# Optimization experiments

Measured on AMD Instinct MI355X. Metric: run time of the kernel, lower is better.

## Reference

```python
import jax, jax.numpy as jnp
import numpy as np

B, T, D_IN, H, D_OUT = 64, 512, 512, 1024, 512

def setup_inputs() -> dict:
    key = jax.random.key(0)
    ks = jax.random.split(key, 8)
    s = 0.02  # weight init scale to keep gates in a sane range
    return {
        "x": jax.random.normal(ks[0], (B, T, D_IN), jnp.float32),
        "hx": jax.random.normal(ks[1], (B, H), jnp.float32) * 0.1,
        "cx": jax.random.normal(ks[2], (B, H), jnp.float32) * 0.1,
        "yx": jax.nn.softmax(jax.random.normal(ks[3], (B, D_OUT), jnp.float32), axis=-1),
        "Wi": jax.random.normal(ks[4], (4 * H, D_IN), jnp.float32) * s,
        "bi": jnp.zeros((4 * H,), jnp.float32),
        "Wh": jax.random.normal(ks[5], (4 * H, H), jnp.float32) * s,
        "bh": jnp.zeros((4 * H,), jnp.float32),
        "Wp": jax.random.normal(ks[6], (4 * H, D_OUT), jnp.float32) * s,
        "bp": jnp.zeros((4 * H,), jnp.float32),
        "Wo": jax.random.normal(ks[7], (D_OUT, H), jnp.float32) * s,
        "bo": jnp.zeros((D_OUT,), jnp.float32),
    }

def reference(x, hx, cx, yx, Wi, bi, Wh, bh, Wp, bp, Wo, bo):
    # Precompute input projections for all timesteps: [T, B, 4H]
    xg = jnp.einsum("btd,gd->tbg", x, Wi) + bi

    def step(carry, xg_t):
        h, c, y = carry
        gates = xg_t + h @ Wh.T + bh + y @ Wp.T + bp  # [B, 4H]
        i_g, f_g, g_g, o_g = jnp.split(gates, 4, axis=-1)
        i_g = jax.nn.sigmoid(i_g)
        f_g = jax.nn.sigmoid(f_g)
        g_g = jnp.tanh(g_g)
        o_g = jax.nn.sigmoid(o_g)
        c_new = f_g * c + i_g * g_g
        h_new = o_g * jnp.tanh(c_new)
        y_new = jax.nn.softmax(h_new @ Wo.T + bo, axis=-1)  # softmax feedback
        return (h_new, c_new, y_new), (h_new, y_new)

    (hT, cT, yT), (h_seq, y_seq) = jax.lax.scan(step, (hx, cx, yx), xg)
    output = jnp.transpose(h_seq, (1, 0, 2))       # [B, T, H]   (batch_first)
    output_peep = jnp.transpose(y_seq, (1, 0, 2))  # [B, T, D_OUT]
    return output, output_peep, hT, cT, yT
```

## Files before the change

### kernel.cpp

```cpp
#include <hip/hip_runtime.h>
#include <math.h>


typedef __bf16 bf16;
typedef bf16  bf16x8 __attribute__((ext_vector_type(8)));
typedef float f32x4  __attribute__((ext_vector_type(4)));
typedef unsigned long long u64;
typedef unsigned int u32;

#define B_    64
#define T_    512
#define DIN_  512
#define H_    1024
#define DOUT_ 512
#define NBLK  256
#define NTHR  512
#define GBLK  64
#define GROWS 16

__device__ __forceinline__ bf16x8 ld8f(const float* __restrict__ p) {
  const float4 a = *(const float4*)p;
  const float4 b = *(const float4*)(p + 4);
  bf16x8 r;
  r[0]=(bf16)a.x; r[1]=(bf16)a.y; r[2]=(bf16)a.z; r[3]=(bf16)a.w;
  r[4]=(bf16)b.x; r[5]=(bf16)b.y; r[6]=(bf16)b.z; r[7]=(bf16)b.w;
  return r;
}

__device__ __forceinline__ float sigm(float x){ return 1.f/(1.f+__expf(-x)); }

__device__ __forceinline__ void st_u64(void* p, u64 v) {
  __hip_atomic_store((u64*)p, v, __ATOMIC_RELAXED, __HIP_MEMORY_SCOPE_AGENT);
}
__device__ __forceinline__ u64 ld_u64(const void* p) {
  return __hip_atomic_load((const u64*)p, __ATOMIC_RELAXED, __HIP_MEMORY_SCOPE_AGENT);
}
__device__ __forceinline__ void st_u32(void* p, u32 v) {
  __hip_atomic_store((u32*)p, v, __ATOMIC_RELAXED, __HIP_MEMORY_SCOPE_AGENT);
}
__device__ __forceinline__ u32 ld_u32(const void* p) {
  return __hip_atomic_load((const u32*)p, __ATOMIC_RELAXED, __HIP_MEMORY_SCOPE_AGENT);
}
__device__ __forceinline__ void st_f32(float* p, float v) {
  __hip_atomic_store(p, v, __ATOMIC_RELAXED, __HIP_MEMORY_SCOPE_AGENT);
}
__device__ __forceinline__ void at_addf(float* p, float v) {
  __hip_atomic_fetch_add(p, v, __ATOMIC_RELAXED, __HIP_MEMORY_SCOPE_AGENT);
}
__device__ __forceinline__ bf16x8 ldh16(const bf16* p) {
  union { u64 q[2]; bf16x8 v; } u;
  u.q[0] = ld_u64(p);
  u.q[1] = ld_u64(p + 4);
  return u.v;
}

__global__ __launch_bounds__(NTHR, 2)
void lstm_kernel(const float* __restrict__ x,  const float* __restrict__ hx,
                 const float* __restrict__ cx, const float* __restrict__ yx,
                 const float* __restrict__ Wi, const float* __restrict__ bi,
                 const float* __restrict__ Wh, const float* __restrict__ bh,
                 const float* __restrict__ Wp, const float* __restrict__ bp,
                 const float* __restrict__ Wo, const float* __restrict__ bo,
                 float* __restrict__ out, char* __restrict__ ws) {
  u32*   flags  = (u32*)ws;
  float* logits = (float*)(ws + 32768);
  bf16*  hbuf   = (bf16*)(ws + 32768 + 4*3*GROWS*DOUT_*4);

  float* out_h  = out;
  float* out_y  = out + (size_t)B_*T_*H_;
  float* out_hT = out_y + (size_t)B_*T_*DOUT_;
  float* out_cT = out_hT + B_*H_;
  float* out_yT = out_cT + B_*H_;

  const int tid  = threadIdx.x;
  const int bid  = blockIdx.x;
  const int g    = bid & 3;
  const int n    = bid >> 2;
  const int w    = tid >> 6;
  const int lane = tid & 63;
  const int quad = lane >> 4;
  const int ln15 = lane & 15;
  const int r0   = g * GROWS;

  u32*   gfl = flags + (size_t)(g * GBLK) * 32;
  float* lgt = logits + (size_t)g * 3 * GROWS * DOUT_;

  __shared__ float lred[8][16][66];
  __shared__ bf16  hstage[16][16];
  __shared__ float lds_rs[2][16];

  bf16* h0 = hbuf;
  bf16* h1 = hbuf + (size_t)B_*H_;

  bf16x8 wfrag[8][4];
  {
    #pragma unroll
    for (int ks = 0; ks < 8; ++ks) {
      #pragma unroll
      for (int ns = 0; ns < 4; ++ns) {
        const int grow = ns*H_ + n*16 + ln15;
        const int kabs = w*256 + ks*32 + quad*8;
        const float* p;
        if      (w < 2) p = Wi + (size_t)grow * DIN_  + kabs;
        else if (w < 6) p = Wh + (size_t)grow * H_    + (kabs - 512);
        else            p = Wp + (size_t)grow * DOUT_ + (kabs - 1536);
        wfrag[ks][ns] = ld8f(p);
      }
    }
  }

  bf16x8 wofrag2[4];
  {
    bf16x8 z;
    #pragma unroll
    for (int j = 0; j < 8; ++j) z[j] = (bf16)0.f;
    #pragma unroll
    for (int m = 0; m < 4; ++m) {
      if (quad < 2)
        wofrag2[m] = ld8f(Wo + (size_t)(w*64 + m*16 + ln15)*H_ + n*16 + quad*8);
      else
        wofrag2[m] = z;
    }
  }

  const int crow = (tid >> 4) & 15;
  const int chl  = tid & 15;
  const int cb   = r0 + crow;
  const int ccol = n*16 + chl;
  float c = 0.f;
  float bias4[4];
  if (tid < 256) {
    c = cx[(size_t)cb * H_ + ccol];
    #pragma unroll
    for (int gg = 0; gg < 4; ++gg) {
      const int grow = gg*H_ + ccol;
      bias4[gg] = bi[grow] + bh[grow] + bp[grow];
    }
  }

  float bo_mine = 0.f;
  if (tid < 128) bo_mine = bo[(n*128 + tid) & (DOUT_ - 1)];

  {
    const int idx = n * NTHR + tid;
    if (idx < GROWS*H_/2) {
      const int row = idx >> 9, c2 = (idx & 511) * 2;
      const float* hp = hx + (size_t)(r0 + row)*H_ + c2;
      union { u32 q; bf16 h[2]; } u;
      u.h[0] = (bf16)hp[0]; u.h[1] = (bf16)hp[1];
      st_u32(h0 + (size_t)(r0 + row)*H_ + c2, u.q);
    }
    if (tid < 128) st_f32(lgt + n*128 + tid, bo_mine);
  }

  u32 ep = 1;
  {
    asm volatile("s_waitcnt vmcnt(0)" ::: "memory");
    __syncthreads();
    if (tid == 0) st_u32(gfl + (size_t)n * 32, ep);
    if (tid < GBLK) {
      const u32* f = gfl + (size_t)tid * 32;
      while (ld_u32(f) < ep) __builtin_amdgcn_s_sleep(1);
    }
    __syncthreads();
  }

  for (int t = 0; t < T_; ++t) {
    bf16*       hbR = (t & 1) ? h1 : h0;
    bf16*       hbW = (t & 1) ? h0 : h1;
    const float* lgtPrev = lgt + (size_t)((t + 2) % 3) * GROWS * DOUT_;
    float*       lgtCur  = lgt + (size_t)(t % 3)       * GROWS * DOUT_;
    float*       lgtNext = lgt + (size_t)((t + 1) % 3) * GROWS * DOUT_;

    f32x4 acc[4];
    #pragma unroll
    for (int j = 0; j < 4; ++j) acc[j] = f32x4{0.f, 0.f, 0.f, 0.f};

    if (w < 2) {
      const float* base = x + ((size_t)(r0 + ln15)*T_ + t)*DIN_ + w*256 + quad*8;
      #pragma unroll
      for (int ks = 0; ks < 8; ++ks) {
        const bf16x8 a = ld8f(base + ks*32);
        #pragma unroll
        for (int ns = 0; ns < 4; ++ns)
          acc[ns] = __builtin_amdgcn_mfma_f32_16x16x32_bf16(a, wfrag[ks][ns], acc[ns], 0,0,0);
      }
    } else if (w < 6) {
      const bf16* base = hbR + (size_t)(r0 + ln15)*H_ + (w-2)*256 + quad*8;
      #pragma unroll
      for (int ks = 0; ks < 8; ++ks) {
        const bf16x8 a = ldh16(base + ks*32);
        #pragma unroll
        for (int ns = 0; ns < 4; ++ns)
          acc[ns] = __builtin_amdgcn_mfma_f32_16x16x32_bf16(a, wfrag[ks][ns], acc[ns], 0,0,0);
      }
    } else {
      float rs = 0.f;
      #pragma unroll
      for (int ks = 0; ks < 8; ++ks) {
        const int col = (w-6)*256 + ks*32 + quad*8;
        float pv[8];
        if (t == 0) {
          const float* yp = yx + (size_t)(r0 + ln15)*DOUT_ + col;
          const float4 a4 = *(const float4*)yp;
          const float4 b4 = *(const float4*)(yp + 4);
          pv[0]=a4.x; pv[1]=a4.y; pv[2]=a4.z; pv[3]=a4.w;
          pv[4]=b4.x; pv[5]=b4.y; pv[6]=b4.z; pv[7]=b4.w;
        } else {
          const float* pp = lgtPrev + ln15*DOUT_ + col;
          #pragma unroll
          for (int u2 = 0; u2 < 4; ++u2) {
            union { u64 q; float f[2]; } ua; ua.q = ld_u64(pp + u2*2);
            pv[u2*2]   = __expf(ua.f[0]);
            pv[u2*2+1] = __expf(ua.f[1]);
          }
        }
        bf16x8 a;
        #pragma unroll
        for (int j = 0; j < 8; ++j) { rs += pv[j]; a[j] = (bf16)pv[j]; }
        #pragma unroll
        for (int ns = 0; ns < 4; ++ns)
          acc[ns] = __builtin_amdgcn_mfma_f32_16x16x32_bf16(a, wfrag[ks][ns], acc[ns], 0,0,0);
      }
      rs += __shfl_xor(rs, 16);
      rs += __shfl_xor(rs, 32);
      if (quad == 0) lds_rs[w-6][ln15] = rs;
    }

    #pragma unroll
    for (int ns = 0; ns < 4; ++ns)
      #pragma unroll
      for (int r = 0; r < 4; ++r)
        lred[w][quad*4 + r][ns*16 + ln15] = acc[ns][r];
    __syncthreads();

    float rinv_y = 1.f;
    if (w >= 6 && t > 0)
      rinv_y = 1.f / (lds_rs[0][ln15] + lds_rs[1][ln15]);

    float hn = 0.f;
    if (tid < 256) {
      const float rsum = lds_rs[0][crow] + lds_rs[1][crow];
      const float rinv = (t == 0) ? 1.f : 1.f / rsum;
      float v[4];
      #pragma unroll
      for (int gg = 0; gg < 4; ++gg) {
        const int cl = gg*16 + chl;
        const float s05 = lred[0][crow][cl] + lred[1][crow][cl] + lred[2][crow][cl]
                        + lred[3][crow][cl] + lred[4][crow][cl] + lred[5][crow][cl];
        const float se  = lred[6][crow][cl] + lred[7][crow][cl];
        v[gg] = s05 + se * rinv + bias4[gg];
      }
      const float ig = sigm(v[0]);
      const float fg = sigm(v[1]);
      const float gv = tanhf(v[2]);
      const float og = sigm(v[3]);
      c = fg * c + ig * gv;
      hn = og * tanhf(c);
      hstage[crow][chl] = (bf16)hn;
    }
    __syncthreads();

    {
      bf16x8 a2;
      #pragma unroll
      for (int j = 0; j < 8; ++j) a2[j] = (bf16)0.f;
      if (quad < 2) a2 = *(const bf16x8*)&hstage[ln15][quad*8];
      #pragma unroll
      for (int m = 0; m < 4; ++m) {
        f32x4 d = f32x4{0.f, 0.f, 0.f, 0.f};
        d = __builtin_amdgcn_mfma_f32_16x16x32_bf16(a2, wofrag2[m], d, 0,0,0);
        #pragma unroll
        for (int r = 0; r < 4; ++r)
          at_addf(lgtCur + (quad*4 + r)*DOUT_ + w*64 + m*16 + ln15, d[r]);
      }
    }

    if (tid < 64) {
      const int row = tid >> 2, c4 = (tid & 3) * 4;
      union { u64 q; bf16 h[4]; } u;
      #pragma unroll
      for (int j = 0; j < 4; ++j) u.h[j] = hstage[row][c4 + j];
      st_u64(hbW + (size_t)(r0 + row)*H_ + n*16 + c4, u.q);
    }
    if (tid < 128) st_f32(lgtNext + n*128 + tid, bo_mine);

    asm volatile("s_waitcnt vmcnt(0)" ::: "memory");
    __syncthreads();
    ++ep;
    if (tid == 0) st_u32(gfl + (size_t)n * 32, ep);

    if (tid < 256) {
      out_h[((size_t)cb * T_ + t) * H_ + ccol] = hn;
      if (t == T_ - 1) {
        out_hT[(size_t)cb * H_ + ccol] = hn;
        out_cT[(size_t)cb * H_ + ccol] = c;
      }
    }
    if (w >= 6 && n < 8 && t > 0) {
      const int col = (w-6)*256 + n*32 + quad*8;
      const float* pp = lgtPrev + ln15*DOUT_ + col;
      float* oy = out_y + ((size_t)(r0 + ln15)*T_ + (t - 1))*DOUT_ + col;
      #pragma unroll
      for (int u2 = 0; u2 < 4; ++u2) {
        union { u64 q; float f[2]; } ua; ua.q = ld_u64(pp + u2*2);
        oy[u2*2]   = __expf(ua.f[0]) * rinv_y;
        oy[u2*2+1] = __expf(ua.f[1]) * rinv_y;
      }
    }

    if (tid < GBLK) {
      const u32* f = gfl + (size_t)tid * 32;
      while (ld_u32(f) < ep) __builtin_amdgcn_s_sleep(1);
    }
    __syncthreads();
  }

  if (n < 8) {
    const float* lp = lgt + (size_t)((T_ + 2) % 3) * GROWS * DOUT_;
    if (w >= 6) {
      float rs = 0.f;
      #pragma unroll
      for (int ks = 0; ks < 8; ++ks) {
        const int col = (w-6)*256 + ks*32 + quad*8;
        const float* pp = lp + ln15*DOUT_ + col;
        #pragma unroll
        for (int u2 = 0; u2 < 4; ++u2) {
          union { u64 q; float f[2]; } ua; ua.q = ld_u64(pp + u2*2);
          rs += __expf(ua.f[0]) + __expf(ua.f[1]);
        }
      }
      rs += __shfl_xor(rs, 16);
      rs += __shfl_xor(rs, 32);
      if (quad == 0) lds_rs[w-6][ln15] = rs;
    }
    __syncthreads();
    if (w >= 6) {
      const float rinv = 1.f / (lds_rs[0][ln15] + lds_rs[1][ln15]);
      const int col = (w-6)*256 + n*32 + quad*8;
      const float* pp = lp + ln15*DOUT_ + col;
      float* oy  = out_y  + ((size_t)(r0 + ln15)*T_ + (T_ - 1))*DOUT_ + col;
      float* oyT = out_yT + (size_t)(r0 + ln15)*DOUT_ + col;
      #pragma unroll
      for (int u2 = 0; u2 < 4; ++u2) {
        union { u64 q; float f[2]; } ua; ua.q = ld_u64(pp + u2*2);
        const float y0 = __expf(ua.f[0]) * rinv;
        const float y1 = __expf(ua.f[1]) * rinv;
        oy[u2*2] = y0;  oy[u2*2+1] = y1;
        oyT[u2*2] = y0; oyT[u2*2+1] = y1;
      }
    }
  }
}

extern "C" void kernel_launch(void* const* d_in, const int* in_sizes, int n_in,
                              void* d_out, int out_size, void* d_ws, size_t ws_size,
                              hipStream_t stream) {
  (void)hipMemsetAsync(d_ws, 0, 32768, stream);
  hipLaunchKernelGGL(lstm_kernel, dim3(NBLK), dim3(NTHR), 0, stream,
                     (const float*)d_in[0],  (const float*)d_in[1],
                     (const float*)d_in[2],  (const float*)d_in[3],
                     (const float*)d_in[4],  (const float*)d_in[5],
                     (const float*)d_in[6],  (const float*)d_in[7],
                     (const float*)d_in[8],  (const float*)d_in[9],
                     (const float*)d_in[10], (const float*)d_in[11],
                     (float*)d_out, (char*)d_ws);
}
```

Before: 7.253 ms.

## Replace atomic logit accumulation with second barrier phase and bf16 exp buffer

Drops the per-step float atomic adds into a shared logits buffer. Each step now has two grid-group barriers: after h is published, every block computes a full-K slice of the output projection for 8 logit columns, exponentiates it, and writes bf16 exp values for the next step's peephole input. The x input projection for the next step is computed early, after the second barrier, to take it off the critical path. The second barrier adds a sync per step, and storing exp values as bf16 instead of fp32 logits lowers the precision of the softmax numerator and its sum.

Measured after the change: 6.384 ms. 1.14x faster.

```diff
diff --git a/kernel.cpp b/kernel.cpp
--- a/kernel.cpp
+++ b/kernel.cpp
@@ -41,12 +41,6 @@
 __device__ __forceinline__ u32 ld_u32(const void* p) {
   return __hip_atomic_load((const u32*)p, __ATOMIC_RELAXED, __HIP_MEMORY_SCOPE_AGENT);
 }
-__device__ __forceinline__ void st_f32(float* p, float v) {
-  __hip_atomic_store(p, v, __ATOMIC_RELAXED, __HIP_MEMORY_SCOPE_AGENT);
-}
-__device__ __forceinline__ void at_addf(float* p, float v) {
-  __hip_atomic_fetch_add(p, v, __ATOMIC_RELAXED, __HIP_MEMORY_SCOPE_AGENT);
-}
 __device__ __forceinline__ bf16x8 ldh16(const bf16* p) {
   union { u64 q[2]; bf16x8 v; } u;
   u.q[0] = ld_u64(p);
@@ -62,9 +56,10 @@
                  const float* __restrict__ Wp, const float* __restrict__ bp,
                  const float* __restrict__ Wo, const float* __restrict__ bo,
                  float* __restrict__ out, char* __restrict__ ws) {
-  u32*   flags  = (u32*)ws;
-  float* logits = (float*)(ws + 32768);
-  bf16*  hbuf   = (bf16*)(ws + 32768 + 4*3*GROWS*DOUT_*4);
+  u32*  flagsA = (u32*)ws;
+  u32*  flagsB = (u32*)(ws + 32768);
+  bf16* hbuf   = (bf16*)(ws + 65536);
+  bf16* ebuf   = (bf16*)(ws + 65536 + (size_t)2*B_*H_*2);
 
   float* out_h  = out;
   float* out_y  = out + (size_t)B_*T_*H_;
@@ -82,8 +77,8 @@
   const int ln15 = lane & 15;
   const int r0   = g * GROWS;
 
-  u32*   gfl = flags + (size_t)(g * GBLK) * 32;
-  float* lgt = logits + (size_t)g * 3 * GROWS * DOUT_;
+  u32* gflA = flagsA + (size_t)(g * GBLK) * 32;
+  u32* gflB = flagsB + (size_t)(g * GBLK) * 32;
 
   __shared__ float lred[8][16][66];
   __shared__ bf16  hstage[16][16];
@@ -109,19 +104,13 @@
     }
   }
 
-  bf16x8 wofrag2[4];
+  bf16x8 wofrag[4];
   {
-    bf16x8 z;
-    #pragma unroll
-    for (int j = 0; j < 8; ++j) z[j] = (bf16)0.f;
-    #pragma unroll
-    for (int m = 0; m < 4; ++m) {
-      if (quad < 2)
-        wofrag2[m] = ld8f(Wo + (size_t)(w*64 + m*16 + ln15)*H_ + n*16 + quad*8);
-      else
-        wofrag2[m] = z;
-    }
-  }
+    #pragma unroll
+    for (int ks = 0; ks < 4; ++ks)
+      wofrag[ks] = ld8f(Wo + (size_t)(n*8 + (ln15 & 7))*H_ + w*128 + ks*32 + quad*8);
+  }
+  const float bo_reg = bo[n*8 + (tid & 7)];
 
   const int crow = (tid >> 4) & 15;
   const int chl  = tid & 15;
@@ -138,9 +127,6 @@
     }
   }
 
-  float bo_mine = 0.f;
-  if (tid < 128) bo_mine = bo[(n*128 + tid) & (DOUT_ - 1)];
-
   {
     const int idx = n * NTHR + tid;
     if (idx < GROWS*H_/2) {
@@ -150,77 +136,80 @@
       u.h[0] = (bf16)hp[0]; u.h[1] = (bf16)hp[1];
       st_u32(h0 + (size_t)(r0 + row)*H_ + c2, u.q);
     }
-    if (tid < 128) st_f32(lgt + n*128 + tid, bo_mine);
-  }
-
-  u32 ep = 1;
-  {
-    asm volatile("s_waitcnt vmcnt(0)" ::: "memory");
-    __syncthreads();
-    if (tid == 0) st_u32(gfl + (size_t)n * 32, ep);
+  }
+
+  f32x4 acc[4];
+  if (w < 2) {
+    #pragma unroll
+    for (int j = 0; j < 4; ++j) acc[j] = f32x4{0.f, 0.f, 0.f, 0.f};
+    const float* base = x + (size_t)(r0 + ln15)*T_*DIN_ + w*256 + quad*8;
+    #pragma unroll
+    for (int ks = 0; ks < 8; ++ks) {
+      const bf16x8 a = ld8f(base + ks*32);
+      #pragma unroll
+      for (int ns = 0; ns < 4; ++ns)
+        acc[ns] = __builtin_amdgcn_mfma_f32_16x16x32_bf16(a, wfrag[ks][ns], acc[ns], 0,0,0);
+    }
+  }
+
+  asm volatile("s_waitcnt vmcnt(0)" ::: "memory");
+  __syncthreads();
+  if (tid == 0) st_u32(gflA + (size_t)n * 32, 1u);
+
+  for (int t = 0; t < T_; ++t) {
+    const bf16* hbR = (t & 1) ? h1 : h0;
+    bf16*       hbW = (t & 1) ? h0 : h1;
+    const bf16* EbR = ebuf + (size_t)((t + 2) % 3) * B_ * DOUT_;
+    bf16*       EbW = ebuf + (size_t)(t % 3)       * B_ * DOUT_;
+
     if (tid < GBLK) {
-      const u32* f = gfl + (size_t)tid * 32;
-      while (ld_u32(f) < ep) __builtin_amdgcn_s_sleep(1);
-    }
-    __syncthreads();
-  }
-
-  for (int t = 0; t < T_; ++t) {
-    bf16*       hbR = (t & 1) ? h1 : h0;
-    bf16*       hbW = (t & 1) ? h0 : h1;
-    const float* lgtPrev = lgt + (size_t)((t + 2) % 3) * GROWS * DOUT_;
-    float*       lgtCur  = lgt + (size_t)(t % 3)       * GROWS * DOUT_;
-    float*       lgtNext = lgt + (size_t)((t + 1) % 3) * GROWS * DOUT_;
-
-    f32x4 acc[4];
-    #pragma unroll
-    for (int j = 0; j < 4; ++j) acc[j] = f32x4{0.f, 0.f, 0.f, 0.f};
-
-    if (w < 2) {
-      const float* base = x + ((size_t)(r0 + ln15)*T_ + t)*DIN_ + w*256 + quad*8;
+      const u32* f = gflA + (size_t)tid * 32;
+      while (ld_u32(f) < (u32)(t + 1)) __builtin_amdgcn_s_sleep(1);
+    }
+    __syncthreads();
+
+    float rinv_y = 1.f;
+
+    if (w >= 2 && w < 6) {
+      #pragma unroll
+      for (int j = 0; j < 4; ++j) acc[j] = f32x4{0.f, 0.f, 0.f, 0.f};
+      const bf16* base = hbR + (size_t)(r0 + ln15)*H_ + (w-2)*256 + quad*8;
       #pragma unroll
       for (int ks = 0; ks < 8; ++ks) {
-        const bf16x8 a = ld8f(base + ks*32);
+        const bf16x8 a = ldh16(base + ks*32);
         #pragma unroll
         for (int ns = 0; ns < 4; ++ns)
           acc[ns] = __builtin_amdgcn_mfma_f32_16x16x32_bf16(a, wfrag[ks][ns], acc[ns], 0,0,0);
       }
-    } else if (w < 6) {
-      const bf16* base = hbR + (size_t)(r0 + ln15)*H_ + (w-2)*256 + quad*8;
-      #pragma unroll
-      for (int ks = 0; ks < 8; ++ks) {
-        const bf16x8 a = ldh16(base + ks*32);
-        #pragma unroll
-        for (int ns = 0; ns < 4; ++ns)
-          acc[ns] = __builtin_amdgcn_mfma_f32_16x16x32_bf16(a, wfrag[ks][ns], acc[ns], 0,0,0);
-      }
-    } else {
+    } else if (w >= 6) {
+      #pragma unroll
+      for (int j = 0; j < 4; ++j) acc[j] = f32x4{0.f, 0.f, 0.f, 0.f};
       float rs = 0.f;
-      #pragma unroll
-      for (int ks = 0; ks < 8; ++ks) {
-        const int col = (w-6)*256 + ks*32 + quad*8;
-        float pv[8];
-        if (t == 0) {
-          const float* yp = yx + (size_t)(r0 + ln15)*DOUT_ + col;
-          const float4 a4 = *(const float4*)yp;
-          const float4 b4 = *(const float4*)(yp + 4);
-          pv[0]=a4.x; pv[1]=a4.y; pv[2]=a4.z; pv[3]=a4.w;
-          pv[4]=b4.x; pv[5]=b4.y; pv[6]=b4.z; pv[7]=b4.w;
-        } else {
-          const float* pp = lgtPrev + ln15*DOUT_ + col;
+      if (t == 0) {
+        const float* yp0 = yx + (size_t)(r0 + ln15)*DOUT_ + (w-6)*256 + quad*8;
+        #pragma unroll
+        for (int ks = 0; ks < 8; ++ks) {
+          const float4 a4 = *(const float4*)(yp0 + ks*32);
+          const float4 b4 = *(const float4*)(yp0 + ks*32 + 4);
+          bf16x8 a;
+          a[0]=(bf16)a4.x; a[1]=(bf16)a4.y; a[2]=(bf16)a4.z; a[3]=(bf16)a4.w;
+          a[4]=(bf16)b4.x; a[5]=(bf16)b4.y; a[6]=(bf16)b4.z; a[7]=(bf16)b4.w;
+          rs += a4.x+a4.y+a4.z+a4.w+b4.x+b4.y+b4.z+b4.w;
           #pragma unroll
-          for (int u2 = 0; u2 < 4; ++u2) {
-            union { u64 q; float f[2]; } ua; ua.q = ld_u64(pp + u2*2);
-            pv[u2*2]   = __expf(ua.f[0]);
-            pv[u2*2+1] = __expf(ua.f[1]);
-          }
+          for (int ns = 0; ns < 4; ++ns)
+            acc[ns] = __builtin_amdgcn_mfma_f32_16x16x32_bf16(a, wfrag[ks][ns], acc[ns], 0,0,0);
         }
-        bf16x8 a;
-        #pragma unroll
-        for (int j = 0; j < 8; ++j) { rs += pv[j]; a[j] = (bf16)pv[j]; }
-        #pragma unroll
-        for (int ns = 0; ns < 4; ++ns)
-          acc[ns] = __builtin_amdgcn_mfma_f32_16x16x32_bf16(a, wfrag[ks][ns], acc[ns], 0,0,0);
+      } else {
+        const bf16* base = EbR + (size_t)(r0 + ln15)*DOUT_ + (w-6)*256 + quad*8;
+        #pragma unroll
+        for (int ks = 0; ks < 8; ++ks) {
+          const bf16x8 a = ldh16(base + ks*32);
+          #pragma unroll
+          for (int j = 0; j < 8; ++j) rs += (float)a[j];
+          #pragma unroll
+          for (int ns = 0; ns < 4; ++ns)
+            acc[ns] = __builtin_amdgcn_mfma_f32_16x16x32_bf16(a, wfrag[ks][ns], acc[ns], 0,0,0);
+        }
       }
       rs += __shfl_xor(rs, 16);
       rs += __shfl_xor(rs, 32);
@@ -234,7 +223,6 @@
         lred[w][quad*4 + r][ns*16 + ln15] = acc[ns][r];
     __syncthreads();
 
-    float rinv_y = 1.f;
     if (w >= 6 && t > 0)
       rinv_y = 1.f / (lds_rs[0][ln15] + lds_rs[1][ln15]);
 
@@ -261,21 +249,6 @@
     }
     __syncthreads();
 
-    {
-      bf16x8 a2;
-      #pragma unroll
-      for (int j = 0; j < 8; ++j) a2[j] = (bf16)0.f;
-      if (quad < 2) a2 = *(const bf16x8*)&hstage[ln15][quad*8];
-      #pragma unroll
-      for (int m = 0; m < 4; ++m) {
-        f32x4 d = f32x4{0.f, 0.f, 0.f, 0.f};
-        d = __builtin_amdgcn_mfma_f32_16x16x32_bf16(a2, wofrag2[m], d, 0,0,0);
-        #pragma unroll
-        for (int r = 0; r < 4; ++r)
-          at_addf(lgtCur + (quad*4 + r)*DOUT_ + w*64 + m*16 + ln15, d[r]);
-      }
-    }
-
     if (tid < 64) {
       const int row = tid >> 2, c4 = (tid & 3) * 4;
       union { u64 q; bf16 h[4]; } u;
@@ -283,12 +256,10 @@
       for (int j = 0; j < 4; ++j) u.h[j] = hstage[row][c4 + j];
       st_u64(hbW + (size_t)(r0 + row)*H_ + n*16 + c4, u.q);
     }
-    if (tid < 128) st_f32(lgtNext + n*128 + tid, bo_mine);
 
     asm volatile("s_waitcnt vmcnt(0)" ::: "memory");
     __syncthreads();
-    ++ep;
-    if (tid == 0) st_u32(gfl + (size_t)n * 32, ep);
+    if (tid == 0) st_u32(gflB + (size_t)n * 32, (u32)(t + 1));
 
     if (tid < 256) {
       out_h[((size_t)cb * T_ + t) * H_ + ccol] = hn;
@@ -297,38 +268,85 @@
         out_cT[(size_t)cb * H_ + ccol] = c;
       }
     }
-    if (w >= 6 && n < 8 && t > 0) {
+
+    if (tid < GBLK) {
+      const u32* f = gflB + (size_t)tid * 32;
+      while (ld_u32(f) < (u32)(t + 1)) __builtin_amdgcn_s_sleep(1);
+    }
+    __syncthreads();
+
+    {
+      f32x4 a2 = f32x4{0.f, 0.f, 0.f, 0.f};
+      const bf16* base = hbW + (size_t)(r0 + ln15)*H_ + w*128 + quad*8;
+      #pragma unroll
+      for (int ks = 0; ks < 4; ++ks) {
+        const bf16x8 af = ldh16(base + ks*32);
+        a2 = __builtin_amdgcn_mfma_f32_16x16x32_bf16(af, wofrag[ks], a2, 0,0,0);
+      }
+      #pragma unroll
+      for (int r = 0; r < 4; ++r)
+        lred[w][quad*4 + r][ln15] = a2[r];
+    }
+    __syncthreads();
+    if (w < 2) {
+      const int row = (tid >> 3) & 15;
+      const int col = tid & 7;
+      float s = bo_reg;
+      #pragma unroll
+      for (int ww = 0; ww < 8; ++ww) s += lred[ww][row][col];
+      const float ee = __expf(s);
+      const float e2 = __shfl_down(ee, 1);
+      if (!(col & 1)) {
+        union { u32 q; bf16 h[2]; } u;
+        u.h[0] = (bf16)ee; u.h[1] = (bf16)e2;
+        st_u32(EbW + (size_t)(r0 + row)*DOUT_ + n*8 + col, u.q);
+      }
+    }
+
+    asm volatile("s_waitcnt vmcnt(0)" ::: "memory");
+    __syncthreads();
+    if (tid == 0) st_u32(gflA + (size_t)n * 32, (u32)(t + 2));
+
+    if (t > 0 && w >= 6 && n < 8) {
       const int col = (w-6)*256 + n*32 + quad*8;
-      const float* pp = lgtPrev + ln15*DOUT_ + col;
+      const bf16x8 ev = ldh16(EbR + (size_t)(r0 + ln15)*DOUT_ + col);
       float* oy = out_y + ((size_t)(r0 + ln15)*T_ + (t - 1))*DOUT_ + col;
-      #pragma unroll
-      for (int u2 = 0; u2 < 4; ++u2) {
-        union { u64 q; float f[2]; } ua; ua.q = ld_u64(pp + u2*2);
-        oy[u2*2]   = __expf(ua.f[0]) * rinv_y;
-        oy[u2*2+1] = __expf(ua.f[1]) * rinv_y;
-      }
-    }
-
-    if (tid < GBLK) {
-      const u32* f = gfl + (size_t)tid * 32;
-      while (ld_u32(f) < ep) __builtin_amdgcn_s_sleep(1);
-    }
-    __syncthreads();
-  }
-
+      float4 o1, o2;
+      o1.x = (float)ev[0]*rinv_y; o1.y = (float)ev[1]*rinv_y;
+      o1.z = (float)ev[2]*rinv_y; o1.w = (float)ev[3]*rinv_y;
+      o2.x = (float)ev[4]*rinv_y; o2.y = (float)ev[5]*rinv_y;
+      o2.z = (float)ev[6]*rinv_y; o2.w = (float)ev[7]*rinv_y;
+      *(float4*)oy = o1; *(float4*)(oy + 4) = o2;
+    }
+    if (w < 2 && t + 1 < T_) {
+      #pragma unroll
+      for (int j = 0; j < 4; ++j) acc[j] = f32x4{0.f, 0.f, 0.f, 0.f};
+      const float* base = x + ((size_t)(r0 + ln15)*T_ + (t + 1))*DIN_ + w*256 + quad*8;
+      #pragma unroll
+      for (int ks = 0; ks < 8; ++ks) {
+        const bf16x8 a = ld8f(base + ks*32);
+        #pragma unroll
+        for (int ns = 0; ns < 4; ++ns)
+          acc[ns] = __builtin_amdgcn_mfma_f32_16x16x32_bf16(a, wfrag[ks][ns], acc[ns], 0,0,0);
+      }
+    }
+  }
+
+  if (tid < GBLK) {
+    const u32* f = gflA + (size_t)tid * 32;
+    while (ld_u32(f) < (u32)(T_ + 1)) __builtin_amdgcn_s_sleep(1);
+  }
+  __syncthreads();
   if (n < 8) {
-    const float* lp = lgt + (size_t)((T_ + 2) % 3) * GROWS * DOUT_;
+    const bf16* eb = ebuf + (size_t)((T_ - 1) % 3) * B_ * DOUT_;
     if (w >= 6) {
       float rs = 0.f;
       #pragma unroll
       for (int ks = 0; ks < 8; ++ks) {
         const int col = (w-6)*256 + ks*32 + quad*8;
-        const float* pp = lp + ln15*DOUT_ + col;
-        #pragma unroll
-        for (int u2 = 0; u2 < 4; ++u2) {
-          union { u64 q; float f[2]; } ua; ua.q = ld_u64(pp + u2*2);
-          rs += __expf(ua.f[0]) + __expf(ua.f[1]);
-        }
+        const bf16x8 ev = ldh16(eb + (size_t)(r0 + ln15)*DOUT_ + col);
+        #pragma unroll
+        for (int j = 0; j < 8; ++j) rs += (float)ev[j];
       }
       rs += __shfl_xor(rs, 16);
       rs += __shfl_xor(rs, 32);
@@ -338,17 +356,16 @@
     if (w >= 6) {
       const float rinv = 1.f / (lds_rs[0][ln15] + lds_rs[1][ln15]);
       const int col = (w-6)*256 + n*32 + quad*8;
-      const float* pp = lp + ln15*DOUT_ + col;
+      const bf16x8 ev = ldh16(eb + (size_t)(r0 + ln15)*DOUT_ + col);
       float* oy  = out_y  + ((size_t)(r0 + ln15)*T_ + (T_ - 1))*DOUT_ + col;
       float* oyT = out_yT + (size_t)(r0 + ln15)*DOUT_ + col;
-      #pragma unroll
-      for (int u2 = 0; u2 < 4; ++u2) {
-        union { u64 q; float f[2]; } ua; ua.q = ld_u64(pp + u2*2);
-        const float y0 = __expf(ua.f[0]) * rinv;
-        const float y1 = __expf(ua.f[1]) * rinv;
-        oy[u2*2] = y0;  oy[u2*2+1] = y1;
-        oyT[u2*2] = y0; oyT[u2*2+1] = y1;
-      }
+      float4 o1, o2;
+      o1.x = (float)ev[0]*rinv; o1.y = (float)ev[1]*rinv;
+      o1.z = (float)ev[2]*rinv; o1.w = (float)ev[3]*rinv;
+      o2.x = (float)ev[4]*rinv; o2.y = (float)ev[5]*rinv;
+      o2.z = (float)ev[6]*rinv; o2.w = (float)ev[7]*rinv;
+      *(float4*)oy  = o1; *(float4*)(oy  + 4) = o2;
+      *(float4*)oyT = o1; *(float4*)(oyT + 4) = o2;
     }
   }
 }
@@ -356,7 +373,7 @@
 extern "C" void kernel_launch(void* const* d_in, const int* in_sizes, int n_in,
                               void* d_out, int out_size, void* d_ws, size_t ws_size,
                               hipStream_t stream) {
-  (void)hipMemsetAsync(d_ws, 0, 32768, stream);
+  (void)hipMemsetAsync(d_ws, 0, 65536, stream);
   hipLaunchKernelGGL(lstm_kernel, dim3(NBLK), dim3(NTHR), 0, stream,
                      (const float*)d_in[0],  (const float*)d_in[1],
                      (const float*)d_in[2],  (const float*)d_in[3],
```
